# Kernel tuning notes

Hardware: AMD Instinct MI355X
Metric: run time of the kernel (lower is better)

## Reference

```python
import jax, jax.numpy as jnp
import numpy as np

E, C, M, H, O = 8, 1024, 2048, 8192, 2048  # experts, capacity, model_dim, hidden, output_dim


def setup_inputs() -> dict:
    key = jax.random.key(0)
    k1, k2, k3, k4, k5 = jax.random.split(key, 5)
    s1 = 1.0 / np.sqrt(M)
    s2 = 1.0 / np.sqrt(H)
    return {
        "x": jax.random.normal(k1, (E, C, M), dtype=jnp.float32),
        "fc1_w": jax.random.normal(k2, (E, H, M), dtype=jnp.float32) * s1,
        "fc1_b": jax.random.normal(k3, (E, H), dtype=jnp.float32) * s1,
        "fc2_w": jax.random.normal(k4, (E, H, O), dtype=jnp.float32) * s2,
        "fc2_b": jax.random.normal(k5, (E, O), dtype=jnp.float32) * s2,
    }


def reference(x, fc1_w, fc1_b, fc2_w, fc2_b):
    # grouped GEMM: per-expert FC1 + bias + ReLU + FC2 + bias
    # x: [E, C, M], fc1_w: [E, H, M], fc2_w: [E, H, O]
    y = jnp.einsum('ecm,ehm->ech', x, fc1_w) + fc1_b[:, None, :]   # [E, C, H]
    y = jax.nn.relu(y)
    y = jnp.einsum('ech,eho->eco', y, fc2_w) + fc2_b[:, None, :]   # [E, C, O]
    return y
```

## Files before the change

kernel.cpp:

```cpp
#include <hip/hip_runtime.h>
#include <hip/hip_bf16.h>
#include <stddef.h>

constexpr int E_ = 8;
constexpr int C_ = 1024;
constexpr int M_ = 2048;
constexpr int H_ = 8192;
constexpr int O_ = 2048;

typedef __bf16 bf16;
typedef __bf16 bf16x4 __attribute__((ext_vector_type(4)));
typedef __bf16 bf16x8 __attribute__((ext_vector_type(8)));
typedef float  f32x4  __attribute__((ext_vector_type(4)));

#define GLOAD16(src, dst)                                                        \
    __builtin_amdgcn_global_load_lds(                                            \
        (const __attribute__((address_space(1))) void*)(src),                    \
        (__attribute__((address_space(3))) void*)(dst), 16, 0, 0)

__global__ __launch_bounds__(256)
void cvt_f32_bf16(const float* __restrict__ in, bf16* __restrict__ out, size_t n)
{
    size_t i = ((size_t)blockIdx.x * blockDim.x + threadIdx.x) * 8;
    const size_t stride = (size_t)gridDim.x * blockDim.x * 8;
    for (; i < n; i += stride) {
        f32x4 v0 = *(const f32x4*)(in + i);
        f32x4 v1 = *(const f32x4*)(in + i + 4);
        bf16x8 o;
#pragma unroll
        for (int j = 0; j < 4; ++j) { o[j] = (bf16)v0[j]; o[j + 4] = (bf16)v1[j]; }
        *(bf16x8*)(out + i) = o;
    }
}

__global__ __launch_bounds__(256)
void transpose_w2(const float* __restrict__ W2, bf16* __restrict__ W2t, int e0)
{
    const int e  = e0 + blockIdx.z;
    const int oo = blockIdx.x;
    const int ho = blockIdx.y;
    const int tid = threadIdx.x;

    __shared__ bf16 t[64][68];

    const float* src = W2 + (size_t)e * H_ * O_ + (size_t)(ho * 64) * O_ + oo * 64;
#pragma unroll
    for (int p = 0; p < 4; ++p) {
        const int h  = p * 16 + (tid >> 4);
        const int o4 = (tid & 15) * 4;
        f32x4 v = *(const f32x4*)(src + (size_t)h * O_ + o4);
#pragma unroll
        for (int q = 0; q < 4; ++q) t[o4 + q][h] = (bf16)v[q];
    }
    __syncthreads();

    bf16* dst = W2t + (size_t)blockIdx.z * O_ * H_ + (size_t)(oo * 64) * H_ + ho * 64;
#pragma unroll
    for (int p = 0; p < 4; ++p) {
        const int o  = p * 16 + (tid >> 4);
        const int h4 = (tid & 15) * 4;
        bf16x4 v = *(const bf16x4*)(&t[o][h4]);
        *(bf16x4*)(dst + (size_t)o * H_ + h4) = v;
    }
}

template<int KDIM, bool RELU_BF16>
__global__ __launch_bounds__(512, 2)
void gemm256(const bf16* __restrict__ A, const bf16* __restrict__ B,
             const float* __restrict__ bias, void* __restrict__ OutP,
             int nBM, int nBN)
{
    extern __shared__ char smem[];
    constexpr int K2  = KDIM * 2;
    constexpr int NKT = KDIM / 32;

    const int tid  = threadIdx.x;
    const int lane = tid & 63;
    const int wid  = tid >> 6;
    const int wr = wid >> 2, wc = wid & 3;
    const int fr = lane & 15, fq = lane >> 4;

    const int nwg = gridDim.x;
    const int cpx = nwg >> 3;
    const int b0  = blockIdx.x;
    const int wg  = (b0 & 7) * cpx + (b0 >> 3);
    const int per_e = nBM * nBN;
    const int e  = wg / per_e;
    const int rr = wg - e * per_e;
    const int bn = rr / nBM;
    const int bm = rr - bn * nBM;
    const int MROWS = nBM * 256;
    const int NROWS = nBN * 256;

    const char* Apan = (const char*)(A + (size_t)e * MROWS * KDIM + (size_t)bm * 256 * KDIM);
    const char* Bpan = (const char*)(B + (size_t)e * NROWS * KDIM + (size_t)bn * 256 * KDIM);

    int off_i[2];
#pragma unroll
    for (int i = 0; i < 2; ++i) {
        int p   = i * 8192 + tid * 16;
        int sub = p >> 10;
        int u   = p & 1023;
        u ^= ((u >> 8) & 3) << 4;
        int row = sub * 16 + (u >> 6);
        off_i[i] = row * K2 + (u & 63);
    }
    const int ao0 = off_i[0], ao1 = off_i[1];
    const int ldso = tid * 16;
    const int laneoff = fr * 64 + ((fq ^ (fr >> 2)) & 3) * 16;

    f32x4 acc[8][4];
#pragma unroll
    for (int m = 0; m < 8; ++m)
#pragma unroll
        for (int n = 0; n < 4; ++n) acc[m][n] = (f32x4){0.f, 0.f, 0.f, 0.f};

    auto stage = [&](int s) {
        char* lb = smem + (s & 3) * 32768;
        const char* ka = Apan + (size_t)s * 64;
        const char* kb = Bpan + (size_t)s * 64;
        GLOAD16(ka + ao0, lb + ldso);
        GLOAD16(ka + ao1, lb + 8192  + ldso);
        GLOAD16(kb + ao0, lb + 16384 + ldso);
        GLOAD16(kb + ao1, lb + 24576 + ldso);
    };

    stage(0); stage(1); stage(2);
    asm volatile("s_waitcnt vmcnt(8)" ::: "memory");
    __builtin_amdgcn_s_barrier();
    __builtin_amdgcn_sched_barrier(0);

    for (int t = 0; t < NKT; ++t) {
        if (t + 3 < NKT) stage(t + 3);

        const char* Ab = smem + (t & 3) * 32768;
        const char* Bb = Ab + 16384;
        bf16x8 av[8], bv[4];
#pragma unroll
        for (int n = 0; n < 4; ++n)
            bv[n] = *(const bf16x8*)(Bb + (wc * 4 + n) * 1024 + laneoff);
#pragma unroll
        for (int m = 0; m < 8; ++m)
            av[m] = *(const bf16x8*)(Ab + (wr * 8 + m) * 1024 + laneoff);

        __builtin_amdgcn_s_setprio(1);
#pragma unroll
        for (int m = 0; m < 8; ++m)
#pragma unroll
            for (int n = 0; n < 4; ++n)
                acc[m][n] = __builtin_amdgcn_mfma_f32_16x16x32_bf16(av[m], bv[n], acc[m][n], 0, 0, 0);
        __builtin_amdgcn_s_setprio(0);

        if (t + 3 < NKT)      asm volatile("s_waitcnt vmcnt(8)" ::: "memory");
        else if (t + 2 < NKT) asm volatile("s_waitcnt vmcnt(4)" ::: "memory");
        else if (t + 1 < NKT) asm volatile("s_waitcnt vmcnt(0)" ::: "memory");
        if (t + 1 < NKT) {
            __builtin_amdgcn_s_barrier();
            __builtin_amdgcn_sched_barrier(0);
        }
    }

    const int gr0 = bm * 256 + wr * 128;
    const int gc0 = bn * 256 + wc * 64;
    if constexpr (RELU_BF16) {
        bf16* Out = (bf16*)OutP;
#pragma unroll
        for (int n = 0; n < 4; ++n) {
            const int col = gc0 + n * 16 + fr;
            const float bb = bias[(size_t)e * NROWS + col];
#pragma unroll
            for (int m = 0; m < 8; ++m)
#pragma unroll
                for (int j = 0; j < 4; ++j) {
                    float v = acc[m][n][j] + bb;
                    v = v > 0.f ? v : 0.f;
                    const int row = gr0 + m * 16 + fq * 4 + j;
                    Out[((size_t)e * MROWS + row) * NROWS + col] = (bf16)v;
                }
        }
    } else {
        float* Out = (float*)OutP;
#pragma unroll
        for (int n = 0; n < 4; ++n) {
            const int col = gc0 + n * 16 + fr;
            const float bb = bias[(size_t)e * NROWS + col];
#pragma unroll
            for (int m = 0; m < 8; ++m)
#pragma unroll
                for (int j = 0; j < 4; ++j) {
                    const int row = gr0 + m * 16 + fq * 4 + j;
                    Out[((size_t)e * MROWS + row) * NROWS + col] = acc[m][n][j] + bb;
                }
        }
    }
}

extern "C" void kernel_launch(void* const* d_in, const int* in_sizes, int n_in,
                              void* d_out, int out_size, void* d_ws, size_t ws_size,
                              hipStream_t stream)
{
    const float* x  = (const float*)d_in[0];
    const float* w1 = (const float*)d_in[1];
    const float* b1 = (const float*)d_in[2];
    const float* w2 = (const float*)d_in[3];
    const float* b2 = (const float*)d_in[4];
    float* out = (float*)d_out;

    (void)hipFuncSetAttribute(reinterpret_cast<const void*>(&gemm256<M_, true>),
                              hipFuncAttributeMaxDynamicSharedMemorySize, 131072);
    (void)hipFuncSetAttribute(reinterpret_cast<const void*>(&gemm256<H_, false>),
                              hipFuncAttributeMaxDynamicSharedMemorySize, 131072);

    const size_t xb_sz  = (size_t)E_ * C_ * M_ * sizeof(bf16);
    const size_t w1b_sz = (size_t)E_ * H_ * M_ * sizeof(bf16);
    const size_t w2t_sz = (size_t)E_ * O_ * H_ * sizeof(bf16);
    const size_t y1_sz  = (size_t)E_ * C_ * H_ * sizeof(bf16);

    if (ws_size >= xb_sz + w1b_sz + w2t_sz + y1_sz) {
        bf16* xb  = (bf16*)d_ws;
        bf16* w1b = (bf16*)((char*)d_ws + xb_sz);
        bf16* w2t = (bf16*)((char*)d_ws + xb_sz + w1b_sz);
        bf16* y1  = (bf16*)((char*)d_ws + xb_sz + w1b_sz + w2t_sz);

        cvt_f32_bf16<<<2048, 256, 0, stream>>>(x,  xb,  (size_t)E_ * C_ * M_);
        cvt_f32_bf16<<<2048, 256, 0, stream>>>(w1, w1b, (size_t)E_ * H_ * M_);
        transpose_w2<<<dim3(O_ / 64, H_ / 64, E_), 256, 0, stream>>>(w2, w2t, 0);

        gemm256<M_, true><<<dim3(8 * 4 * (H_ / 256)), 512, 131072, stream>>>(
            xb, w1b, b1, y1, 4, H_ / 256);
        gemm256<H_, false><<<dim3(8 * 4 * (O_ / 256)), 512, 131072, stream>>>(
            y1, w2t, b2, out, 4, O_ / 256);
    } else {
        bf16* xb  = (bf16*)d_ws;
        bf16* w1b = (bf16*)((char*)d_ws + xb_sz / E_);
        bf16* w2t = (bf16*)((char*)d_ws + (xb_sz + w1b_sz) / E_);
        bf16* y1  = (bf16*)((char*)d_ws + (xb_sz + w1b_sz + w2t_sz) / E_);
        for (int e = 0; e < E_; ++e) {
            cvt_f32_bf16<<<512, 256, 0, stream>>>(x + (size_t)e * C_ * M_,  xb,  (size_t)C_ * M_);
            cvt_f32_bf16<<<2048, 256, 0, stream>>>(w1 + (size_t)e * H_ * M_, w1b, (size_t)H_ * M_);
            transpose_w2<<<dim3(O_ / 64, H_ / 64, 1), 256, 0, stream>>>(w2, w2t, e);
            gemm256<M_, true><<<dim3(4 * (H_ / 256)), 512, 131072, stream>>>(
                xb, w1b, b1 + (size_t)e * H_, y1, 4, H_ / 256);
            gemm256<H_, false><<<dim3(4 * (O_ / 256)), 512, 131072, stream>>>(
                y1, w2t, b2 + (size_t)e * O_, out + (size_t)e * C_ * O_, 4, O_ / 256);
        }
    }
}
```

Baseline: 897.1 us.

## Restructure GEMM main loop into 64-wide K tiles with interleaved quarter-stage pipelining

Replaces the 4-stage, 32-wide K pipeline with a double-buffered layout of 64-wide K tiles, each split into four 16KB components loaded as halves. The main loop now interleaves partial LDS fragment loads, quarter-block MFMA groups and the next tile's global-to-LDS loads, with barriers between them, in a ping-pong schedule across two buffers. A new XOR swizzle keeps LDS reads conflict-free. The aim is finer overlap of memory traffic with MFMA and fewer waits per K step, at the cost of many more barriers and more intricate vmcnt accounting.

```diff
diff --git a/kernel.cpp b/kernel.cpp
--- a/kernel.cpp
+++ b/kernel.cpp
@@ -17,6 +17,11 @@
     __builtin_amdgcn_global_load_lds(                                            \
         (const __attribute__((address_space(1))) void*)(src),                    \
         (__attribute__((address_space(3))) void*)(dst), 16, 0, 0)
+
+#define BARRIER()  __builtin_amdgcn_s_barrier()
+#define LGKM0()    do { asm volatile("s_waitcnt lgkmcnt(0)" ::: "memory");       \
+                        __builtin_amdgcn_sched_barrier(0); } while (0)
+#define VMCNT(n)   asm volatile("s_waitcnt vmcnt(" #n ")" ::: "memory")
 
 __global__ __launch_bounds__(256)
 void cvt_f32_bf16(const float* __restrict__ in, bf16* __restrict__ out, size_t n)
@@ -72,7 +77,7 @@
 {
     extern __shared__ char smem[];
     constexpr int K2  = KDIM * 2;
-    constexpr int NKT = KDIM / 32;
+    constexpr int NIT = KDIM / 128;
 
     const int tid  = threadIdx.x;
     const int lane = tid & 63;
@@ -95,68 +100,122 @@
     const char* Apan = (const char*)(A + (size_t)e * MROWS * KDIM + (size_t)bm * 256 * KDIM);
     const char* Bpan = (const char*)(B + (size_t)e * NROWS * KDIM + (size_t)bn * 256 * KDIM);
 
-    int off_i[2];
-#pragma unroll
-    for (int i = 0; i < 2; ++i) {
-        int p   = i * 8192 + tid * 16;
-        int sub = p >> 10;
-        int u   = p & 1023;
-        u ^= ((u >> 8) & 3) << 4;
-        int row = sub * 16 + (u >> 6);
-        off_i[i] = row * K2 + (u & 63);
-    }
-    const int ao0 = off_i[0], ao1 = off_i[1];
-    const int ldso = tid * 16;
-    const int laneoff = fr * 64 + ((fq ^ (fr >> 2)) & 3) * 16;
-
+    const int r0  = tid >> 3;
+    const int wsw = ((tid & 7) << 4) ^ ((r0 & 7) << 4);
+
+    auto stage_half = [&](int g, int comp) {
+        char* lds = smem + (g & 1) * 65536 + comp * 16384 + tid * 16;
+        const char* pan = (comp < 2) ? Apan : Bpan;
+        const char* src = pan + (size_t)(((comp & 1) << 7) + r0) * K2
+                              + (size_t)g * 128 + wsw;
+        GLOAD16(src, lds);
+        GLOAD16(src + (size_t)64 * K2, lds + 8192);
+    };
+
+    const int frq = fr & 7;
+    const int cA0 = ((fq    ) ^ frq) << 4;
+    const int cA1 = ((4 | fq) ^ frq) << 4;
+    const int aoff = wr * 16384 + fr * 128;
+    const int boff = 32768 + (wc >> 1) * 16384 + (wc & 1) * 8192 + fr * 128;
+
+    bf16x8 av[4][2];
+    bf16x8 bv[4][2];
     f32x4 acc[8][4];
 #pragma unroll
     for (int m = 0; m < 8; ++m)
 #pragma unroll
         for (int n = 0; n < 4; ++n) acc[m][n] = (f32x4){0.f, 0.f, 0.f, 0.f};
 
-    auto stage = [&](int s) {
-        char* lb = smem + (s & 3) * 32768;
-        const char* ka = Apan + (size_t)s * 64;
-        const char* kb = Bpan + (size_t)s * 64;
-        GLOAD16(ka + ao0, lb + ldso);
-        GLOAD16(ka + ao1, lb + 8192  + ldso);
-        GLOAD16(kb + ao0, lb + 16384 + ldso);
-        GLOAD16(kb + ao1, lb + 24576 + ldso);
+    auto loadA = [&](const char* base, int mh) {
+#pragma unroll
+        for (int mm = 0; mm < 4; ++mm) {
+            const char* p = base + aoff + (mh * 4 + mm) * 2048;
+            av[mm][0] = *(const bf16x8*)(p + cA0);
+            av[mm][1] = *(const bf16x8*)(p + cA1);
+        }
     };
-
-    stage(0); stage(1); stage(2);
-    asm volatile("s_waitcnt vmcnt(8)" ::: "memory");
-    __builtin_amdgcn_s_barrier();
-    __builtin_amdgcn_sched_barrier(0);
-
-    for (int t = 0; t < NKT; ++t) {
-        if (t + 3 < NKT) stage(t + 3);
-
-        const char* Ab = smem + (t & 3) * 32768;
-        const char* Bb = Ab + 16384;
-        bf16x8 av[8], bv[4];
-#pragma unroll
-        for (int n = 0; n < 4; ++n)
-            bv[n] = *(const bf16x8*)(Bb + (wc * 4 + n) * 1024 + laneoff);
-#pragma unroll
-        for (int m = 0; m < 8; ++m)
-            av[m] = *(const bf16x8*)(Ab + (wr * 8 + m) * 1024 + laneoff);
-
+    auto loadB = [&](const char* base, int nh) {
+#pragma unroll
+        for (int nn = 0; nn < 2; ++nn) {
+            const char* p = base + boff + (nh * 2 + nn) * 2048;
+            bv[nh * 2 + nn][0] = *(const bf16x8*)(p + cA0);
+            bv[nh * 2 + nn][1] = *(const bf16x8*)(p + cA1);
+        }
+    };
+    auto mmaq = [&](int mh, int nh) {
         __builtin_amdgcn_s_setprio(1);
 #pragma unroll
-        for (int m = 0; m < 8; ++m)
-#pragma unroll
-            for (int n = 0; n < 4; ++n)
-                acc[m][n] = __builtin_amdgcn_mfma_f32_16x16x32_bf16(av[m], bv[n], acc[m][n], 0, 0, 0);
+        for (int mm = 0; mm < 4; ++mm)
+#pragma unroll
+            for (int nn = 0; nn < 2; ++nn) {
+                const int m = mh * 4 + mm, n = nh * 2 + nn;
+                acc[m][n] = __builtin_amdgcn_mfma_f32_16x16x32_bf16(av[mm][0], bv[n][0], acc[m][n], 0, 0, 0);
+                acc[m][n] = __builtin_amdgcn_mfma_f32_16x16x32_bf16(av[mm][1], bv[n][1], acc[m][n], 0, 0, 0);
+            }
         __builtin_amdgcn_s_setprio(0);
-
-        if (t + 3 < NKT)      asm volatile("s_waitcnt vmcnt(8)" ::: "memory");
-        else if (t + 2 < NKT) asm volatile("s_waitcnt vmcnt(4)" ::: "memory");
-        else if (t + 1 < NKT) asm volatile("s_waitcnt vmcnt(0)" ::: "memory");
-        if (t + 1 < NKT) {
-            __builtin_amdgcn_s_barrier();
-            __builtin_amdgcn_sched_barrier(0);
+    };
+
+    stage_half(0, 2); stage_half(0, 3); stage_half(0, 0); stage_half(0, 1);
+    stage_half(1, 2); stage_half(1, 3);
+    VMCNT(4);
+    BARRIER();
+
+    for (int t = 0; t < NIT; ++t) {
+        const bool nl = (t + 1 < NIT);
+        const char* d0b = smem;
+        const char* d1b = smem + 65536;
+        const int ga = 2 * t + 1;
+        const int gb = 2 * t + 2;
+        const int gc = 2 * t + 3;
+
+        loadB(d0b, 0); loadA(d0b, 0);
+        stage_half(ga, 0);
+        BARRIER(); LGKM0();
+        mmaq(0, 0);
+        BARRIER();
+
+        loadB(d0b, 1);
+        stage_half(ga, 1);
+        BARRIER(); LGKM0();
+        mmaq(0, 1);
+        BARRIER();
+
+        loadA(d0b, 1);
+        if (nl) stage_half(gb, 2);
+        BARRIER(); LGKM0();
+        mmaq(1, 1);
+        BARRIER();
+
+        if (nl) stage_half(gb, 3);
+        BARRIER(); LGKM0();
+        mmaq(1, 0);
+        if (nl) { VMCNT(4); } else { VMCNT(0); }
+        BARRIER();
+
+        loadB(d1b, 0); loadA(d1b, 0);
+        if (nl) stage_half(gb, 0);
+        BARRIER(); LGKM0();
+        mmaq(0, 0);
+        BARRIER();
+
+        loadB(d1b, 1);
+        if (nl) stage_half(gb, 1);
+        BARRIER(); LGKM0();
+        mmaq(0, 1);
+        BARRIER();
+
+        loadA(d1b, 1);
+        if (nl) stage_half(gc, 2);
+        BARRIER(); LGKM0();
+        mmaq(1, 1);
+        BARRIER();
+
+        if (nl) stage_half(gc, 3);
+        BARRIER(); LGKM0();
+        mmaq(1, 0);
+        if (nl) {
+            VMCNT(4);
+            BARRIER();
         }
     }
 
```

Result: faster. 798.4 us (-11.0%).
